# Kernel tuning notes

Measured on AMD Instinct MI355X. Metric: run time of the kernel, lower is better.

The kernel has to match this reference:

```python
import jax, jax.numpy as jnp
import numpy as np

B, S, H, NH, L, NS = 8, 4096, 768, 12, 2, 64
DH = H // NH
EPS = 1e-12


def _layer_norm(x, g, b):
    mu = jnp.mean(x, axis=-1, keepdims=True)
    var = jnp.mean((x - mu) ** 2, axis=-1, keepdims=True)
    return (x - mu) / jnp.sqrt(var + EPS) * g + b


def setup_inputs() -> dict:
    key = jax.random.key(0)
    ks = jax.random.split(key, 8)
    # sentence index per token: 64 equal contiguous sentences; position 0 is [CLS] in sentence 0
    sent_ind = jnp.broadcast_to((jnp.arange(S, dtype=jnp.int32) * NS) // S, (B, S)).astype(jnp.int32)
    start_layer = jax.random.normal(ks[0], (B, S, H), dtype=jnp.float32)
    init = lambda k, shape: (jax.random.normal(k, shape, dtype=jnp.float32) * 0.02)
    return {
        "sent_ind": sent_ind,
        "start_layer": start_layer,
        "Wq": init(ks[1], (L, H, H)), "bq": jnp.zeros((L, H), jnp.float32),
        "Wk": init(ks[2], (L, H, H)), "bk": jnp.zeros((L, H), jnp.float32),
        "Wv": init(ks[3], (L, H, H)), "bv": jnp.zeros((L, H), jnp.float32),
        "Wo": init(ks[4], (L, H, H)), "bo": jnp.zeros((L, H), jnp.float32),
        "ln_g": jnp.ones((L, H), jnp.float32), "ln_b": jnp.zeros((L, H), jnp.float32),
    }


def reference(sent_ind, start_layer, Wq, bq, Wk, bk, Wv, bv, Wo, bo, ln_g, ln_b):
    # ---- segment-mean pooling by sentence index (vectorized replacement of the python loops) ----
    onehot = (sent_ind[..., None] == jnp.arange(NS, dtype=sent_ind.dtype)).astype(start_layer.dtype)  # [B,S,NS]
    # the first [CLS] token is excluded from sentence 0's mean
    onehot = onehot.at[:, 0, :].set(0.0)
    sums = jnp.einsum('bsn,bsd->bnd', onehot, start_layer)          # [B,NS,H]
    counts = jnp.sum(onehot, axis=1)                                 # [B,NS]
    x = sums / counts[..., None]                                     # graph_vectors [B,NS,H]

    # ---- GAT layers: BertSelfAttention + GATSelfOutput(dense->gelu->LayerNorm), dropout=eval ----
    scale = 1.0 / (DH ** 0.5)
    for i in range(L):
        q = (x @ Wq[i] + bq[i]).reshape(B, NS, NH, DH)
        k = (x @ Wk[i] + bk[i]).reshape(B, NS, NH, DH)
        v = (x @ Wv[i] + bv[i]).reshape(B, NS, NH, DH)
        scores = jnp.einsum('bqhd,bkhd->bhqk', q, k) * scale
        probs = jax.nn.softmax(scores, axis=-1)
        ctx = jnp.einsum('bhqk,bkhd->bqhd', probs, v).reshape(B, NS, H)
        h = jax.nn.gelu(ctx @ Wo[i] + bo[i], approximate=False)
        x = _layer_norm(h, ln_g[i], ln_b[i])
    return x
```

## Files before the change

kernel.cpp:

```cpp
#include <hip/hip_runtime.h>
#include <hip/hip_bf16.h>

constexpr int cB  = 8;
constexpr int cS  = 4096;
constexpr int cH  = 768;
constexpr int cNH = 12;
constexpr int cL  = 2;
constexpr int cNS = 64;
constexpr int cDH = 64;
constexpr int cM  = cB * cNS;

typedef __attribute__((ext_vector_type(8))) short bf16x8;
typedef __attribute__((ext_vector_type(4))) float f32x4;

union PrepShared {
    struct { int cnt; int list[cS]; float ps[192][4]; } p;
    float T[2][64][65];
};

__global__ __launch_bounds__(512) void prep_kernel(
    const int* __restrict__ sent_ind, const float* __restrict__ sl,
    __hip_bfloat16* __restrict__ xb,
    const float* __restrict__ Wq, const float* __restrict__ Wk,
    const float* __restrict__ Wv, const float* __restrict__ Wo,
    __hip_bfloat16* __restrict__ wt)
{
    __shared__ PrepShared sh;
    int tid = threadIdx.x;

    if (blockIdx.x < (unsigned)cM) {
        int bn = blockIdx.x;
        int b = bn >> 6, n = bn & (cNS - 1);
        if (tid == 0) sh.p.cnt = 0;
        __syncthreads();
        const int* si = sent_ind + (size_t)b * cS;
        for (int s = tid; s < cS; s += 512)
            if (s != 0 && si[s] == n) { int p = atomicAdd(&sh.p.cnt, 1); sh.p.list[p] = s; }
        __syncthreads();
        int c = sh.p.cnt;
        int grp = tid >> 8;
        int t   = tid & 255;
        int c0 = c >> 1;
        int lo = grp ? c0 : 0;
        int hi = grp ? c  : c0;
        float s0 = 0.f, s1 = 0.f, s2 = 0.f, s3 = 0.f;
        if (t < 192) {
            const float* bbase = sl + (size_t)b * cS * cH;
            int col = t * 4;
            float4 a0 = {0.f, 0.f, 0.f, 0.f};
            float4 a1 = {0.f, 0.f, 0.f, 0.f};
            float4 a2 = {0.f, 0.f, 0.f, 0.f};
            float4 a3 = {0.f, 0.f, 0.f, 0.f};
            int i = lo;
            for (; i + 4 <= hi; i += 4) {
                float4 r0 = *(const float4*)(bbase + (size_t)sh.p.list[i + 0] * cH + col);
                float4 r1 = *(const float4*)(bbase + (size_t)sh.p.list[i + 1] * cH + col);
                float4 r2 = *(const float4*)(bbase + (size_t)sh.p.list[i + 2] * cH + col);
                float4 r3 = *(const float4*)(bbase + (size_t)sh.p.list[i + 3] * cH + col);
                a0.x += r0.x; a0.y += r0.y; a0.z += r0.z; a0.w += r0.w;
                a1.x += r1.x; a1.y += r1.y; a1.z += r1.z; a1.w += r1.w;
                a2.x += r2.x; a2.y += r2.y; a2.z += r2.z; a2.w += r2.w;
                a3.x += r3.x; a3.y += r3.y; a3.z += r3.z; a3.w += r3.w;
            }
            for (; i < hi; ++i) {
                float4 r0 = *(const float4*)(bbase + (size_t)sh.p.list[i] * cH + col);
                a0.x += r0.x; a0.y += r0.y; a0.z += r0.z; a0.w += r0.w;
            }
            s0 = a0.x + a1.x + a2.x + a3.x;
            s1 = a0.y + a1.y + a2.y + a3.y;
            s2 = a0.z + a1.z + a2.z + a3.z;
            s3 = a0.w + a1.w + a2.w + a3.w;
        }
        if (grp == 1 && t < 192) {
            sh.p.ps[t][0] = s0; sh.p.ps[t][1] = s1;
            sh.p.ps[t][2] = s2; sh.p.ps[t][3] = s3;
        }
        __syncthreads();
        if (grp == 0 && t < 192) {
            float inv = 1.0f / (float)c;
            __hip_bfloat16* xr = xb + (size_t)bn * cH + t * 4;
            xr[0] = __float2bfloat16((s0 + sh.p.ps[t][0]) * inv);
            xr[1] = __float2bfloat16((s1 + sh.p.ps[t][1]) * inv);
            xr[2] = __float2bfloat16((s2 + sh.p.ps[t][2]) * inv);
            xr[3] = __float2bfloat16((s3 + sh.p.ps[t][3]) * inv);
        }
    } else {
        int sub = tid >> 8;
        int t   = tid & 255;
        int bi = (blockIdx.x - cM) * 2 + sub;
        int bx = bi % 12, by = (bi / 12) % 12, mat = bi / 144;
        int layer = mat >> 2, which = mat & 3;
        const float* W = (which == 0 ? Wq : which == 1 ? Wk : which == 2 ? Wv : Wo)
                         + (size_t)layer * cH * cH;
        int k0 = by * 64, n0 = bx * 64;
        int r = t >> 2, cb = (t & 3) * 16;
        #pragma unroll
        for (int u = 0; u < 4; ++u) {
            float4 w4 = *(const float4*)(W + (size_t)(k0 + r) * cH + n0 + cb + u * 4);
            sh.T[sub][r][cb + u * 4 + 0] = w4.x; sh.T[sub][r][cb + u * 4 + 1] = w4.y;
            sh.T[sub][r][cb + u * 4 + 2] = w4.z; sh.T[sub][r][cb + u * 4 + 3] = w4.w;
        }
        __syncthreads();
        int nn = t >> 2, kseg = (t & 3) * 16;
        __hip_bfloat16 tmp[16] __attribute__((aligned(16)));
        #pragma unroll
        for (int j = 0; j < 16; ++j)
            tmp[j] = __float2bfloat16(sh.T[sub][kseg + j][nn]);
        __hip_bfloat16* dst = wt + ((size_t)mat * cH + n0 + nn) * cH + k0 + kseg;
        *(bf16x8*)(dst)     = *(const bf16x8*)(tmp);
        *(bf16x8*)(dst + 8) = *(const bf16x8*)(tmp + 8);
    }
}

struct AttnShared {
    float QP[cNS][cDH + 4];
    float Ks[cNS][cDH + 4];
    float Vt[cDH][cNS + 4];
};

__global__ __launch_bounds__(256) void qkvattn_kernel(
    const __hip_bfloat16* __restrict__ x_bf,
    const __hip_bfloat16* __restrict__ wqkv,
    const float* __restrict__ bq, const float* __restrict__ bk,
    const float* __restrict__ bv,
    __hip_bfloat16* __restrict__ ctx_bf)
{
    __shared__ AttnShared sh;
    int tid = threadIdx.x;
    int lane = tid & 63, wave = tid >> 6;
    int l15 = lane & 15, q4 = lane >> 4;
    int b = blockIdx.x / cNH, hh = blockIdx.x % cNH;

    const __hip_bfloat16* Arow[4];
    #pragma unroll
    for (int m = 0; m < 4; ++m)
        Arow[m] = x_bf + (size_t)(b * 64 + m * 16 + l15) * cH + q4 * 8;
    const __hip_bfloat16* Brow[3];
    int cmat[3], cnt_[3];
    #pragma unroll
    for (int j = 0; j < 3; ++j) {
        int c = wave * 3 + j;
        cmat[j] = c >> 2; cnt_[j] = c & 3;
        Brow[j] = wqkv + (size_t)cmat[j] * cH * cH
                       + (size_t)(hh * 64 + cnt_[j] * 16 + l15) * cH + q4 * 8;
    }

    f32x4 acc[3][4];
    #pragma unroll
    for (int j = 0; j < 3; ++j)
        #pragma unroll
        for (int m = 0; m < 4; ++m) acc[j][m] = (f32x4){0.f, 0.f, 0.f, 0.f};

    #pragma unroll 4
    for (int k0 = 0; k0 < cH; k0 += 32) {
        bf16x8 a[4], bb8[3];
        #pragma unroll
        for (int m = 0; m < 4; ++m) a[m] = *(const bf16x8*)(Arow[m] + k0);
        #pragma unroll
        for (int j = 0; j < 3; ++j) bb8[j] = *(const bf16x8*)(Brow[j] + k0);
        #pragma unroll
        for (int j = 0; j < 3; ++j)
            #pragma unroll
            for (int m = 0; m < 4; ++m)
                acc[j][m] = __builtin_amdgcn_mfma_f32_16x16x32_bf16(a[m], bb8[j], acc[j][m], 0, 0, 0);
    }

    const float scale = 0.125f;
    #pragma unroll
    for (int j = 0; j < 3; ++j) {
        int mat = cmat[j], nt = cnt_[j];
        int col_d = nt * 16 + l15;
        int col_g = hh * 64 + col_d;
        float bias = (mat == 0 ? bq : mat == 1 ? bk : bv)[col_g];
        #pragma unroll
        for (int m = 0; m < 4; ++m) {
            #pragma unroll
            for (int r = 0; r < 4; ++r) {
                int row_s = m * 16 + q4 * 4 + r;
                float v = acc[j][m][r] + bias;
                if (mat == 0)      sh.QP[row_s][col_d] = v * scale;
                else if (mat == 1) sh.Ks[row_s][col_d] = v;
                else               sh.Vt[col_d][row_s] = v;
            }
        }
    }
    __syncthreads();

    int tx = tid & 15, ty = tid >> 4;
    float accs[4][4] = {};
    for (int d = 0; d < cDH; d += 4) {
        float4 qv[4], kv[4];
        #pragma unroll
        for (int i = 0; i < 4; ++i) qv[i] = *(const float4*)&sh.QP[ty * 4 + i][d];
        #pragma unroll
        for (int j = 0; j < 4; ++j) kv[j] = *(const float4*)&sh.Ks[tx + j * 16][d];
        #pragma unroll
        for (int i = 0; i < 4; ++i)
            #pragma unroll
            for (int j = 0; j < 4; ++j)
                accs[i][j] += qv[i].x * kv[j].x + qv[i].y * kv[j].y +
                              qv[i].z * kv[j].z + qv[i].w * kv[j].w;
    }
    __syncthreads();
    #pragma unroll
    for (int i = 0; i < 4; ++i)
        #pragma unroll
        for (int j = 0; j < 4; ++j)
            sh.QP[ty * 4 + i][tx + j * 16] = accs[i][j];
    __syncthreads();

    {
        int row = tid >> 2, jq = tid & 3;
        float e[16];
        float m = -1e30f;
        #pragma unroll
        for (int c = 0; c < 16; ++c) { e[c] = sh.QP[row][jq * 16 + c]; m = fmaxf(m, e[c]); }
        m = fmaxf(m, __shfl_xor(m, 1));
        m = fmaxf(m, __shfl_xor(m, 2));
        float s = 0.f;
        #pragma unroll
        for (int c = 0; c < 16; ++c) { e[c] = __expf(e[c] - m); s += e[c]; }
        s += __shfl_xor(s, 1);
        s += __shfl_xor(s, 2);
        float inv = 1.0f / s;
        #pragma unroll
        for (int c = 0; c < 16; ++c) sh.QP[row][jq * 16 + c] = e[c] * inv;
    }
    __syncthreads();

    float acco[4][4] = {};
    for (int c = 0; c < cNS; c += 4) {
        float4 p4[4], vt4[4];
        #pragma unroll
        for (int i = 0; i < 4; ++i) p4[i] = *(const float4*)&sh.QP[ty * 4 + i][c];
        #pragma unroll
        for (int j = 0; j < 4; ++j) vt4[j] = *(const float4*)&sh.Vt[tx + j * 16][c];
        #pragma unroll
        for (int i = 0; i < 4; ++i)
            #pragma unroll
            for (int j = 0; j < 4; ++j)
                acco[i][j] += p4[i].x * vt4[j].x + p4[i].y * vt4[j].y +
                              p4[i].z * vt4[j].z + p4[i].w * vt4[j].w;
    }
    size_t base = ((size_t)b * cNS) * cH + hh * cDH;
    #pragma unroll
    for (int i = 0; i < 4; ++i)
        #pragma unroll
        for (int j = 0; j < 4; ++j)
            ctx_bf[base + (size_t)(ty * 4 + i) * cH + tx + j * 16] =
                __float2bfloat16(acco[i][j]);
}

__global__ __launch_bounds__(256) void ogemm_kernel(
    const __hip_bfloat16* __restrict__ A,
    const __hip_bfloat16* __restrict__ Wt,
    const float* __restrict__ bias,
    __hip_bfloat16* __restrict__ C)
{
    int lane = threadIdx.x & 63;
    int wave = threadIdx.x >> 6;
    int l15 = lane & 15, q4 = lane >> 4;
    int m0 = blockIdx.y * 64 + wave * 16;
    int n0 = blockIdx.x * 32;

    const __hip_bfloat16* Arow = A  + (size_t)(m0 + l15) * cH + q4 * 8;
    const __hip_bfloat16* Wr0  = Wt + (size_t)(n0 + l15) * cH + q4 * 8;
    const __hip_bfloat16* Wr1  = Wr0 + (size_t)16 * cH;

    f32x4 acc0 = {0.f, 0.f, 0.f, 0.f};
    f32x4 acc1 = {0.f, 0.f, 0.f, 0.f};
    #pragma unroll 8
    for (int k0 = 0; k0 < cH; k0 += 32) {
        bf16x8 a  = *(const bf16x8*)(Arow + k0);
        bf16x8 b0 = *(const bf16x8*)(Wr0 + k0);
        bf16x8 b1 = *(const bf16x8*)(Wr1 + k0);
        acc0 = __builtin_amdgcn_mfma_f32_16x16x32_bf16(a, b0, acc0, 0, 0, 0);
        acc1 = __builtin_amdgcn_mfma_f32_16x16x32_bf16(a, b1, acc1, 0, 0, 0);
    }
    #pragma unroll
    for (int nt = 0; nt < 2; ++nt) {
        const f32x4 acc = nt == 0 ? acc0 : acc1;
        int col = n0 + nt * 16 + l15;
        float bv = bias[col];
        #pragma unroll
        for (int r = 0; r < 4; ++r) {
            float v = acc[r] + bv;
            v = 0.5f * v * (1.0f + erff(v * 0.70710678118654752f));
            C[(size_t)(m0 + q4 * 4 + r) * cH + col] = __float2bfloat16(v);
        }
    }
}

__global__ __launch_bounds__(256) void ln_kernel(
    const __hip_bfloat16* __restrict__ h, const float* __restrict__ g,
    const float* __restrict__ bb, __hip_bfloat16* __restrict__ xb,
    float* __restrict__ outf)
{
    int row = blockIdx.x;
    const __hip_bfloat16* r = h + (size_t)row * cH;
    int tid = threadIdx.x;
    float v0 = __bfloat162float(r[tid]);
    float v1 = __bfloat162float(r[tid + 256]);
    float v2 = __bfloat162float(r[tid + 512]);
    float s = v0 + v1 + v2;
    __shared__ float red[4];
    #pragma unroll
    for (int o = 32; o; o >>= 1) s += __shfl_xor(s, o);
    if ((tid & 63) == 0) red[tid >> 6] = s;
    __syncthreads();
    float mu = (red[0] + red[1] + red[2] + red[3]) * (1.0f / 768.0f);
    float d0 = v0 - mu, d1 = v1 - mu, d2 = v2 - mu;
    float ss = d0 * d0 + d1 * d1 + d2 * d2;
    __syncthreads();
    #pragma unroll
    for (int o = 32; o; o >>= 1) ss += __shfl_xor(ss, o);
    if ((tid & 63) == 0) red[tid >> 6] = ss;
    __syncthreads();
    float var = (red[0] + red[1] + red[2] + red[3]) * (1.0f / 768.0f);
    float inv = rsqrtf(var + 1e-12f);
    float o0 = d0 * inv * g[tid]       + bb[tid];
    float o1 = d1 * inv * g[tid + 256] + bb[tid + 256];
    float o2 = d2 * inv * g[tid + 512] + bb[tid + 512];
    __hip_bfloat16* xr = xb + (size_t)row * cH;
    xr[tid]       = __float2bfloat16(o0);
    xr[tid + 256] = __float2bfloat16(o1);
    xr[tid + 512] = __float2bfloat16(o2);
    if (outf) {
        float* orow = outf + (size_t)row * cH;
        orow[tid] = o0; orow[tid + 256] = o1; orow[tid + 512] = o2;
    }
}

extern "C" void kernel_launch(void* const* d_in, const int* in_sizes, int n_in,
                              void* d_out, int out_size, void* d_ws, size_t ws_size,
                              hipStream_t stream) {
    const int*   sent_ind = (const int*)d_in[0];
    const float* start    = (const float*)d_in[1];
    const float* Wq = (const float*)d_in[2];
    const float* bq = (const float*)d_in[3];
    const float* Wk = (const float*)d_in[4];
    const float* bk = (const float*)d_in[5];
    const float* Wv = (const float*)d_in[6];
    const float* bv = (const float*)d_in[7];
    const float* Wo = (const float*)d_in[8];
    const float* bo = (const float*)d_in[9];
    const float* ln_g = (const float*)d_in[10];
    const float* ln_b = (const float*)d_in[11];
    float* out = (float*)d_out;

    char* w = (char*)d_ws;
    __hip_bfloat16* wt     = (__hip_bfloat16*)w;
    __hip_bfloat16* x_bf   = (__hip_bfloat16*)(w + 9437184);
    __hip_bfloat16* ctx_bf = (__hip_bfloat16*)(w + 9437184 + 786432);
    __hip_bfloat16* hb     = (__hip_bfloat16*)(w + 9437184 + 2 * 786432);

    prep_kernel<<<cM + 576, 512, 0, stream>>>(sent_ind, start, x_bf,
                                              Wq, Wk, Wv, Wo, wt);

    for (int i = 0; i < cL; ++i) {
        const __hip_bfloat16* wqkv = wt + (size_t)(i * 4) * cH * cH;
        const __hip_bfloat16* wto  = wt + (size_t)(i * 4 + 3) * cH * cH;
        qkvattn_kernel<<<cB * cNH, 256, 0, stream>>>(
            x_bf, wqkv, bq + (size_t)i * cH, bk + (size_t)i * cH, bv + (size_t)i * cH,
            ctx_bf);
        ogemm_kernel<<<dim3(24, 8), 256, 0, stream>>>(
            ctx_bf, wto, bo + (size_t)i * cH, hb);
        ln_kernel<<<cM, 256, 0, stream>>>(
            hb, ln_g + (size_t)i * cH, ln_b + (size_t)i * cH,
            x_bf, (i == cL - 1) ? out : nullptr);
    }
}
```

Baseline: 285.1 us.

## Split QKV projection from attention and use MFMA for attention matmuls

The fused QKV+attention kernel (96 blocks) is split into a QKV GEMM kernel with 288 blocks that uses register double-buffered loads, plus a separate attention kernel that computes QK^T and PV with bf16 MFMA instead of scalar FP32 loops. The prep kernel also moves to 768 threads, splitting the pooling reduction four ways and transposing three weight tiles per block. This aims to raise GPU occupancy and cut attention ALU time. It costs an extra kernel launch, a round trip of Q/K/V through global memory, and bf16 rounding of probabilities.

Result: no change. 283.1 us (-0.7%).

```diff
diff --git a/kernel.cpp b/kernel.cpp
--- a/kernel.cpp
+++ b/kernel.cpp
@@ -13,12 +13,17 @@
 typedef __attribute__((ext_vector_type(8))) short bf16x8;
 typedef __attribute__((ext_vector_type(4))) float f32x4;
 
+__device__ __forceinline__ unsigned short f2b(float f) {
+    __hip_bfloat16 h = __float2bfloat16(f);
+    return *(unsigned short*)&h;
+}
+
 union PrepShared {
-    struct { int cnt; int list[cS]; float ps[192][4]; } p;
-    float T[2][64][65];
+    struct { int cnt; int list[cS]; float ps[3][192][4]; } p;
+    float T[3][64][65];
 };
 
-__global__ __launch_bounds__(512) void prep_kernel(
+__global__ __launch_bounds__(768) void prep_kernel(
     const int* __restrict__ sent_ind, const float* __restrict__ sl,
     __hip_bfloat16* __restrict__ xb,
     const float* __restrict__ Wq, const float* __restrict__ Wk,
@@ -34,60 +39,61 @@
         if (tid == 0) sh.p.cnt = 0;
         __syncthreads();
         const int* si = sent_ind + (size_t)b * cS;
-        for (int s = tid; s < cS; s += 512)
+        for (int s = tid; s < cS; s += 768)
             if (s != 0 && si[s] == n) { int p = atomicAdd(&sh.p.cnt, 1); sh.p.list[p] = s; }
         __syncthreads();
         int c = sh.p.cnt;
-        int grp = tid >> 8;
-        int t   = tid & 255;
-        int c0 = c >> 1;
-        int lo = grp ? c0 : 0;
-        int hi = grp ? c  : c0;
-        float s0 = 0.f, s1 = 0.f, s2 = 0.f, s3 = 0.f;
-        if (t < 192) {
-            const float* bbase = sl + (size_t)b * cS * cH;
-            int col = t * 4;
-            float4 a0 = {0.f, 0.f, 0.f, 0.f};
-            float4 a1 = {0.f, 0.f, 0.f, 0.f};
-            float4 a2 = {0.f, 0.f, 0.f, 0.f};
-            float4 a3 = {0.f, 0.f, 0.f, 0.f};
-            int i = lo;
-            for (; i + 4 <= hi; i += 4) {
-                float4 r0 = *(const float4*)(bbase + (size_t)sh.p.list[i + 0] * cH + col);
-                float4 r1 = *(const float4*)(bbase + (size_t)sh.p.list[i + 1] * cH + col);
-                float4 r2 = *(const float4*)(bbase + (size_t)sh.p.list[i + 2] * cH + col);
-                float4 r3 = *(const float4*)(bbase + (size_t)sh.p.list[i + 3] * cH + col);
-                a0.x += r0.x; a0.y += r0.y; a0.z += r0.z; a0.w += r0.w;
-                a1.x += r1.x; a1.y += r1.y; a1.z += r1.z; a1.w += r1.w;
-                a2.x += r2.x; a2.y += r2.y; a2.z += r2.z; a2.w += r2.w;
-                a3.x += r3.x; a3.y += r3.y; a3.z += r3.z; a3.w += r3.w;
-            }
-            for (; i < hi; ++i) {
-                float4 r0 = *(const float4*)(bbase + (size_t)sh.p.list[i] * cH + col);
-                a0.x += r0.x; a0.y += r0.y; a0.z += r0.z; a0.w += r0.w;
-            }
-            s0 = a0.x + a1.x + a2.x + a3.x;
-            s1 = a0.y + a1.y + a2.y + a3.y;
-            s2 = a0.z + a1.z + a2.z + a3.z;
-            s3 = a0.w + a1.w + a2.w + a3.w;
-        }
-        if (grp == 1 && t < 192) {
-            sh.p.ps[t][0] = s0; sh.p.ps[t][1] = s1;
-            sh.p.ps[t][2] = s2; sh.p.ps[t][3] = s3;
+        int grp = tid / 192;
+        int t   = tid % 192;
+        int qtr = c >> 2;
+        int lo = grp * qtr;
+        int hi = (grp == 3) ? c : lo + qtr;
+        const float* bbase = sl + (size_t)b * cS * cH;
+        int col = t * 4;
+        float4 a0 = {0.f, 0.f, 0.f, 0.f};
+        float4 a1 = {0.f, 0.f, 0.f, 0.f};
+        float4 a2 = {0.f, 0.f, 0.f, 0.f};
+        float4 a3 = {0.f, 0.f, 0.f, 0.f};
+        int i = lo;
+        for (; i + 4 <= hi; i += 4) {
+            float4 r0 = *(const float4*)(bbase + (size_t)sh.p.list[i + 0] * cH + col);
+            float4 r1 = *(const float4*)(bbase + (size_t)sh.p.list[i + 1] * cH + col);
+            float4 r2 = *(const float4*)(bbase + (size_t)sh.p.list[i + 2] * cH + col);
+            float4 r3 = *(const float4*)(bbase + (size_t)sh.p.list[i + 3] * cH + col);
+            a0.x += r0.x; a0.y += r0.y; a0.z += r0.z; a0.w += r0.w;
+            a1.x += r1.x; a1.y += r1.y; a1.z += r1.z; a1.w += r1.w;
+            a2.x += r2.x; a2.y += r2.y; a2.z += r2.z; a2.w += r2.w;
+            a3.x += r3.x; a3.y += r3.y; a3.z += r3.z; a3.w += r3.w;
+        }
+        for (; i < hi; ++i) {
+            float4 r0 = *(const float4*)(bbase + (size_t)sh.p.list[i] * cH + col);
+            a0.x += r0.x; a0.y += r0.y; a0.z += r0.z; a0.w += r0.w;
+        }
+        float s0 = a0.x + a1.x + a2.x + a3.x;
+        float s1 = a0.y + a1.y + a2.y + a3.y;
+        float s2 = a0.z + a1.z + a2.z + a3.z;
+        float s3 = a0.w + a1.w + a2.w + a3.w;
+        if (grp) {
+            sh.p.ps[grp - 1][t][0] = s0; sh.p.ps[grp - 1][t][1] = s1;
+            sh.p.ps[grp - 1][t][2] = s2; sh.p.ps[grp - 1][t][3] = s3;
         }
         __syncthreads();
-        if (grp == 0 && t < 192) {
+        if (grp == 0) {
             float inv = 1.0f / (float)c;
-            __hip_bfloat16* xr = xb + (size_t)bn * cH + t * 4;
-            xr[0] = __float2bfloat16((s0 + sh.p.ps[t][0]) * inv);
-            xr[1] = __float2bfloat16((s1 + sh.p.ps[t][1]) * inv);
-            xr[2] = __float2bfloat16((s2 + sh.p.ps[t][2]) * inv);
-            xr[3] = __float2bfloat16((s3 + sh.p.ps[t][3]) * inv);
+            s0 += sh.p.ps[0][t][0] + sh.p.ps[1][t][0] + sh.p.ps[2][t][0];
+            s1 += sh.p.ps[0][t][1] + sh.p.ps[1][t][1] + sh.p.ps[2][t][1];
+            s2 += sh.p.ps[0][t][2] + sh.p.ps[1][t][2] + sh.p.ps[2][t][2];
+            s3 += sh.p.ps[0][t][3] + sh.p.ps[1][t][3] + sh.p.ps[2][t][3];
+            __hip_bfloat16* xr = xb + (size_t)bn * cH + col;
+            xr[0] = __float2bfloat16(s0 * inv);
+            xr[1] = __float2bfloat16(s1 * inv);
+            xr[2] = __float2bfloat16(s2 * inv);
+            xr[3] = __float2bfloat16(s3 * inv);
         }
     } else {
         int sub = tid >> 8;
         int t   = tid & 255;
-        int bi = (blockIdx.x - cM) * 2 + sub;
+        int bi = (blockIdx.x - cM) * 3 + sub;
         int bx = bi % 12, by = (bi / 12) % 12, mat = bi / 144;
         int layer = mat >> 2, which = mat & 3;
         const float* W = (which == 0 ? Wq : which == 1 ? Wk : which == 2 ? Wv : Wo)
@@ -112,101 +118,113 @@
     }
 }
 
-struct AttnShared {
-    float QP[cNS][cDH + 4];
-    float Ks[cNS][cDH + 4];
-    float Vt[cDH][cNS + 4];
-};
-
-__global__ __launch_bounds__(256) void qkvattn_kernel(
+__global__ __launch_bounds__(256) void qkv_kernel(
     const __hip_bfloat16* __restrict__ x_bf,
     const __hip_bfloat16* __restrict__ wqkv,
     const float* __restrict__ bq, const float* __restrict__ bk,
     const float* __restrict__ bv,
-    __hip_bfloat16* __restrict__ ctx_bf)
-{
-    __shared__ AttnShared sh;
+    __hip_bfloat16* __restrict__ q_bf, __hip_bfloat16* __restrict__ k_bf,
+    __hip_bfloat16* __restrict__ v_bf)
+{
     int tid = threadIdx.x;
     int lane = tid & 63, wave = tid >> 6;
     int l15 = lane & 15, q4 = lane >> 4;
-    int b = blockIdx.x / cNH, hh = blockIdx.x % cNH;
-
-    const __hip_bfloat16* Arow[4];
-    #pragma unroll
-    for (int m = 0; m < 4; ++m)
-        Arow[m] = x_bf + (size_t)(b * 64 + m * 16 + l15) * cH + q4 * 8;
-    const __hip_bfloat16* Brow[3];
-    int cmat[3], cnt_[3];
-    #pragma unroll
-    for (int j = 0; j < 3; ++j) {
-        int c = wave * 3 + j;
-        cmat[j] = c >> 2; cnt_[j] = c & 3;
-        Brow[j] = wqkv + (size_t)cmat[j] * cH * cH
-                       + (size_t)(hh * 64 + cnt_[j] * 16 + l15) * cH + q4 * 8;
-    }
-
-    f32x4 acc[3][4];
-    #pragma unroll
-    for (int j = 0; j < 3; ++j)
-        #pragma unroll
-        for (int m = 0; m < 4; ++m) acc[j][m] = (f32x4){0.f, 0.f, 0.f, 0.f};
-
+    int mb = blockIdx.x & 7;
+    int nb = blockIdx.x >> 3;
+    int mat = nb / 12, hh = nb % 12;
+
+    const __hip_bfloat16* Arow = x_bf
+        + (size_t)(mb * 64 + wave * 16 + l15) * cH + q4 * 8;
+    const __hip_bfloat16* Brow = wqkv + (size_t)mat * cH * cH
+        + (size_t)(hh * 64 + l15) * cH + q4 * 8;
+
+    f32x4 acc[4];
+    #pragma unroll
+    for (int nt = 0; nt < 4; ++nt) acc[nt] = (f32x4){0.f, 0.f, 0.f, 0.f};
+
+    bf16x8 a, bw[4], an, bn[4];
+    a = *(const bf16x8*)(Arow);
+    #pragma unroll
+    for (int nt = 0; nt < 4; ++nt)
+        bw[nt] = *(const bf16x8*)(Brow + (size_t)nt * 16 * cH);
     #pragma unroll 4
     for (int k0 = 0; k0 < cH; k0 += 32) {
-        bf16x8 a[4], bb8[3];
-        #pragma unroll
-        for (int m = 0; m < 4; ++m) a[m] = *(const bf16x8*)(Arow[m] + k0);
-        #pragma unroll
-        for (int j = 0; j < 3; ++j) bb8[j] = *(const bf16x8*)(Brow[j] + k0);
-        #pragma unroll
-        for (int j = 0; j < 3; ++j)
+        if (k0 + 32 < cH) {
+            an = *(const bf16x8*)(Arow + k0 + 32);
             #pragma unroll
-            for (int m = 0; m < 4; ++m)
-                acc[j][m] = __builtin_amdgcn_mfma_f32_16x16x32_bf16(a[m], bb8[j], acc[j][m], 0, 0, 0);
-    }
-
-    const float scale = 0.125f;
-    #pragma unroll
-    for (int j = 0; j < 3; ++j) {
-        int mat = cmat[j], nt = cnt_[j];
-        int col_d = nt * 16 + l15;
-        int col_g = hh * 64 + col_d;
-        float bias = (mat == 0 ? bq : mat == 1 ? bk : bv)[col_g];
-        #pragma unroll
-        for (int m = 0; m < 4; ++m) {
+            for (int nt = 0; nt < 4; ++nt)
+                bn[nt] = *(const bf16x8*)(Brow + (size_t)nt * 16 * cH + k0 + 32);
+        }
+        #pragma unroll
+        for (int nt = 0; nt < 4; ++nt)
+            acc[nt] = __builtin_amdgcn_mfma_f32_16x16x32_bf16(a, bw[nt], acc[nt], 0, 0, 0);
+        a = an;
+        #pragma unroll
+        for (int nt = 0; nt < 4; ++nt) bw[nt] = bn[nt];
+    }
+
+    const float* bias = mat == 0 ? bq : mat == 1 ? bk : bv;
+    __hip_bfloat16* dst = (mat == 0 ? q_bf : mat == 1 ? k_bf : v_bf)
+                          + (size_t)(mb * cNH + hh) * 4096;
+    float qs = (mat == 0) ? 0.125f : 1.0f;
+    #pragma unroll
+    for (int nt = 0; nt < 4; ++nt) {
+        int col = nt * 16 + l15;
+        float bv_ = bias[hh * 64 + col];
+        #pragma unroll
+        for (int r = 0; r < 4; ++r) {
+            int s = wave * 16 + q4 * 4 + r;
+            dst[(size_t)s * 64 + col] = __float2bfloat16((acc[nt][r] + bv_) * qs);
+        }
+    }
+}
+
+struct Attn2Shared {
+    float S[cNS][cNS + 4];
+    unsigned short Vt[cDH][cNS + 8];
+    unsigned short P[cNS][cNS + 8];
+};
+
+__global__ __launch_bounds__(256) void attn2_kernel(
+    const __hip_bfloat16* __restrict__ q_bf,
+    const __hip_bfloat16* __restrict__ k_bf,
+    const __hip_bfloat16* __restrict__ v_bf,
+    __hip_bfloat16* __restrict__ ctx_bf)
+{
+    __shared__ Attn2Shared sh;
+    int tid = threadIdx.x;
+    int lane = tid & 63, wave = tid >> 6;
+    int l15 = lane & 15, q4 = lane >> 4;
+    int bh = blockIdx.x, b = bh / cNH, h = bh % cNH;
+    const __hip_bfloat16* qp = q_bf + (size_t)bh * 4096;
+    const __hip_bfloat16* kp = k_bf + (size_t)bh * 4096;
+    const __hip_bfloat16* vp = v_bf + (size_t)bh * 4096;
+
+    #pragma unroll
+    for (int i = 0; i < 2; ++i) {
+        int idx = tid + i * 256;
+        int s = idx >> 3, c0 = (idx & 7) * 8;
+        bf16x8 v8 = *(const bf16x8*)(vp + (size_t)s * 64 + c0);
+        #pragma unroll
+        for (int j = 0; j < 8; ++j)
+            sh.Vt[c0 + j][s] = (unsigned short)v8[j];
+    }
+
+    {
+        bf16x8 aq0 = *(const bf16x8*)(qp + (size_t)(wave * 16 + l15) * 64 + q4 * 8);
+        bf16x8 aq1 = *(const bf16x8*)(qp + (size_t)(wave * 16 + l15) * 64 + 32 + q4 * 8);
+        #pragma unroll
+        for (int ct = 0; ct < 4; ++ct) {
+            bf16x8 bk0 = *(const bf16x8*)(kp + (size_t)(ct * 16 + l15) * 64 + q4 * 8);
+            bf16x8 bk1 = *(const bf16x8*)(kp + (size_t)(ct * 16 + l15) * 64 + 32 + q4 * 8);
+            f32x4 sc = (f32x4){0.f, 0.f, 0.f, 0.f};
+            sc = __builtin_amdgcn_mfma_f32_16x16x32_bf16(aq0, bk0, sc, 0, 0, 0);
+            sc = __builtin_amdgcn_mfma_f32_16x16x32_bf16(aq1, bk1, sc, 0, 0, 0);
             #pragma unroll
-            for (int r = 0; r < 4; ++r) {
-                int row_s = m * 16 + q4 * 4 + r;
-                float v = acc[j][m][r] + bias;
-                if (mat == 0)      sh.QP[row_s][col_d] = v * scale;
-                else if (mat == 1) sh.Ks[row_s][col_d] = v;
-                else               sh.Vt[col_d][row_s] = v;
-            }
-        }
-    }
-    __syncthreads();
-
-    int tx = tid & 15, ty = tid >> 4;
-    float accs[4][4] = {};
-    for (int d = 0; d < cDH; d += 4) {
-        float4 qv[4], kv[4];
-        #pragma unroll
-        for (int i = 0; i < 4; ++i) qv[i] = *(const float4*)&sh.QP[ty * 4 + i][d];
-        #pragma unroll
-        for (int j = 0; j < 4; ++j) kv[j] = *(const float4*)&sh.Ks[tx + j * 16][d];
-        #pragma unroll
-        for (int i = 0; i < 4; ++i)
-            #pragma unroll
-            for (int j = 0; j < 4; ++j)
-                accs[i][j] += qv[i].x * kv[j].x + qv[i].y * kv[j].y +
-                              qv[i].z * kv[j].z + qv[i].w * kv[j].w;
-    }
-    __syncthreads();
-    #pragma unroll
-    for (int i = 0; i < 4; ++i)
-        #pragma unroll
-        for (int j = 0; j < 4; ++j)
-            sh.QP[ty * 4 + i][tx + j * 16] = accs[i][j];
+            for (int r = 0; r < 4; ++r)
+                sh.S[wave * 16 + q4 * 4 + r][ct * 16 + l15] = sc[r];
+        }
+    }
     __syncthreads();
 
     {
@@ -214,7 +232,7 @@
         float e[16];
         float m = -1e30f;
         #pragma unroll
-        for (int c = 0; c < 16; ++c) { e[c] = sh.QP[row][jq * 16 + c]; m = fmaxf(m, e[c]); }
+        for (int c = 0; c < 16; ++c) { e[c] = sh.S[row][jq * 16 + c]; m = fmaxf(m, e[c]); }
         m = fmaxf(m, __shfl_xor(m, 1));
         m = fmaxf(m, __shfl_xor(m, 2));
         float s = 0.f;
@@ -224,31 +242,28 @@
         s += __shfl_xor(s, 2);
         float inv = 1.0f / s;
         #pragma unroll
-        for (int c = 0; c < 16; ++c) sh.QP[row][jq * 16 + c] = e[c] * inv;
-    }
-    __syncthreads();
-
-    float acco[4][4] = {};
-    for (int c = 0; c < cNS; c += 4) {
-        float4 p4[4], vt4[4];
-        #pragma unroll
-        for (int i = 0; i < 4; ++i) p4[i] = *(const float4*)&sh.QP[ty * 4 + i][c];
-        #pragma unroll
-        for (int j = 0; j < 4; ++j) vt4[j] = *(const float4*)&sh.Vt[tx + j * 16][c];
-        #pragma unroll
-        for (int i = 0; i < 4; ++i)
+        for (int c = 0; c < 16; ++c) sh.P[row][jq * 16 + c] = f2b(e[c] * inv);
+    }
+    __syncthreads();
+
+    {
+        bf16x8 ap0 = *(const bf16x8*)&sh.P[wave * 16 + l15][q4 * 8];
+        bf16x8 ap1 = *(const bf16x8*)&sh.P[wave * 16 + l15][32 + q4 * 8];
+        #pragma unroll
+        for (int dt = 0; dt < 4; ++dt) {
+            bf16x8 bv0 = *(const bf16x8*)&sh.Vt[dt * 16 + l15][q4 * 8];
+            bf16x8 bv1 = *(const bf16x8*)&sh.Vt[dt * 16 + l15][32 + q4 * 8];
+            f32x4 o = (f32x4){0.f, 0.f, 0.f, 0.f};
+            o = __builtin_amdgcn_mfma_f32_16x16x32_bf16(ap0, bv0, o, 0, 0, 0);
+            o = __builtin_amdgcn_mfma_f32_16x16x32_bf16(ap1, bv1, o, 0, 0, 0);
             #pragma unroll
-            for (int j = 0; j < 4; ++j)
-                acco[i][j] += p4[i].x * vt4[j].x + p4[i].y * vt4[j].y +
-                              p4[i].z * vt4[j].z + p4[i].w * vt4[j].w;
-    }
-    size_t base = ((size_t)b * cNS) * cH + hh * cDH;
-    #pragma unroll
-    for (int i = 0; i < 4; ++i)
-        #pragma unroll
-        for (int j = 0; j < 4; ++j)
-            ctx_bf[base + (size_t)(ty * 4 + i) * cH + tx + j * 16] =
-                __float2bfloat16(acco[i][j]);
+            for (int r = 0; r < 4; ++r) {
+                int q = wave * 16 + q4 * 4 + r;
+                ctx_bf[(size_t)(b * cNS + q) * cH + h * cDH + dt * 16 + l15] =
+                    __float2bfloat16(o[r]);
+            }
+        }
+    }
 }
 
 __global__ __launch_bounds__(256) void ogemm_kernel(
@@ -349,20 +364,25 @@
     float* out = (float*)d_out;
 
     char* w = (char*)d_ws;
+    const size_t MH = 786432;
     __hip_bfloat16* wt     = (__hip_bfloat16*)w;
     __hip_bfloat16* x_bf   = (__hip_bfloat16*)(w + 9437184);
-    __hip_bfloat16* ctx_bf = (__hip_bfloat16*)(w + 9437184 + 786432);
-    __hip_bfloat16* hb     = (__hip_bfloat16*)(w + 9437184 + 2 * 786432);
-
-    prep_kernel<<<cM + 576, 512, 0, stream>>>(sent_ind, start, x_bf,
+    __hip_bfloat16* ctx_bf = (__hip_bfloat16*)(w + 9437184 + MH);
+    __hip_bfloat16* hb     = (__hip_bfloat16*)(w + 9437184 + 2 * MH);
+    __hip_bfloat16* q_bf   = (__hip_bfloat16*)(w + 9437184 + 3 * MH);
+    __hip_bfloat16* k_bf   = (__hip_bfloat16*)(w + 9437184 + 4 * MH);
+    __hip_bfloat16* v_bf   = (__hip_bfloat16*)(w + 9437184 + 5 * MH);
+
+    prep_kernel<<<cM + 384, 768, 0, stream>>>(sent_ind, start, x_bf,
                                               Wq, Wk, Wv, Wo, wt);
 
     for (int i = 0; i < cL; ++i) {
         const __hip_bfloat16* wqkv = wt + (size_t)(i * 4) * cH * cH;
         const __hip_bfloat16* wto  = wt + (size_t)(i * 4 + 3) * cH * cH;
-        qkvattn_kernel<<<cB * cNH, 256, 0, stream>>>(
+        qkv_kernel<<<288, 256, 0, stream>>>(
             x_bf, wqkv, bq + (size_t)i * cH, bk + (size_t)i * cH, bv + (size_t)i * cH,
-            ctx_bf);
+            q_bf, k_bf, v_bf);
+        attn2_kernel<<<cB * cNH, 256, 0, stream>>>(q_bf, k_bf, v_bf, ctx_bf);
         ogemm_kernel<<<dim3(24, 8), 256, 0, stream>>>(
             ctx_bf, wto, bo + (size_t)i * cH, hb);
         ln_kernel<<<cM, 256, 0, stream>>>(
```
